# Optimization experiments

Measured on AMD Instinct MI355X. Metric: run time of the kernel, lower is better.

Reference implementation:

```python
import jax, jax.numpy as jnp
import numpy as np

N_NODES = 50000
N_EDGES = 800000
IN_DIM = 256
HID = 32
HEADS = 8
OUT_DIM = 16
NEG_SLOPE = 0.2


def setup_inputs() -> dict:
    key = jax.random.key(0)
    ks = jax.random.split(key, 12)
    s = 0.05
    return {
        "emb": jax.random.normal(ks[0], (N_NODES, IN_DIM), jnp.float32),
        "src": jax.random.randint(ks[1], (N_EDGES,), 0, N_NODES),
        "dst": jax.random.randint(ks[2], (N_EDGES,), 0, N_NODES),
        "W1": jax.random.normal(ks[3], (IN_DIM, HEADS * HID), jnp.float32) * s,
        "attn_l1": jax.random.normal(ks[4], (HEADS, HID), jnp.float32) * s,
        "attn_r1": jax.random.normal(ks[5], (HEADS, HID), jnp.float32) * s,
        "bias1": jax.random.normal(ks[6], (HEADS * HID,), jnp.float32) * s,
        "W2": jax.random.normal(ks[7], (HEADS * HID, OUT_DIM), jnp.float32) * s,
        "attn_l2": jax.random.normal(ks[8], (1, OUT_DIM), jnp.float32) * s,
        "attn_r2": jax.random.normal(ks[9], (1, OUT_DIM), jnp.float32) * s,
        "bias2": jax.random.normal(ks[10], (OUT_DIM,), jnp.float32) * s,
    }


def gat_conv(x, src, dst, W, attn_l, attn_r, bias, n_heads, d_out):
    # x: [N, F_in] -> per-head projection h: [N, H, D]
    n = x.shape[0]
    h = (x @ W).reshape(n, n_heads, d_out)
    el = jnp.sum(h * attn_l, axis=-1)  # [N, H]
    er = jnp.sum(h * attn_r, axis=-1)  # [N, H]
    # edge scores with LeakyReLU (DGL negative_slope=0.2)
    e = jax.nn.leaky_relu(el[src] + er[dst], NEG_SLOPE)  # [E, H]
    # edge softmax over incoming edges of each destination node
    m = jax.ops.segment_max(e, dst, num_segments=n)  # [N, H]
    ee = jnp.exp(e - m[dst])
    denom = jax.ops.segment_sum(ee, dst, num_segments=n)  # [N, H]
    alpha = ee / denom[dst]  # [E, H]
    # weighted scatter-sum aggregation
    out = jax.ops.segment_sum(h[src] * alpha[:, :, None], dst, num_segments=n)  # [N, H, D]
    return out + bias.reshape(1, n_heads, d_out)


def reference(emb, src, dst, W1, attn_l1, attn_r1, bias1, W2, attn_l2, attn_r2, bias2):
    h = gat_conv(emb, src, dst, W1, attn_l1, attn_r1, bias1, HEADS, HID)  # [N, 8, 32]
    h = jax.nn.elu(h.reshape(N_NODES, HEADS * HID))  # [N, 256]
    out = gat_conv(h, src, dst, W2, attn_l2, attn_r2, bias2, 1, OUT_DIM)  # [N, 1, 16]
    return jnp.squeeze(out, axis=1)  # [N, 16]
```

## Files before the change

### kernel.cpp

```cpp
#include <hip/hip_runtime.h>
#include <math.h>

#define N_NODES 50000
#define N_EDGES 800000
#define NEG_SLOPE 0.2f

typedef __attribute__((ext_vector_type(8))) short bf16x8;
typedef __attribute__((ext_vector_type(4))) float f32x4;
typedef __attribute__((ext_vector_type(4))) _Float16 half4;

__device__ inline unsigned short f32_to_bf16_rn(float x) {
    unsigned u = __builtin_bit_cast(unsigned, x);
    unsigned r = u + 0x7fffu + ((u >> 16) & 1u);
    return (unsigned short)(r >> 16);
}
__device__ inline float bf16_bits_to_f32(unsigned short h) {
    unsigned u = ((unsigned)h) << 16;
    return __builtin_bit_cast(float, u);
}
__device__ inline void load_lds16(const void* g, void* l) {
    __builtin_amdgcn_global_load_lds(
        (const __attribute__((address_space(1))) void*)g,
        (__attribute__((address_space(3))) void*)l, 16, 0, 0);
}


__global__ void count_deg(const int* __restrict__ dst, int* __restrict__ deg) {
    int i = blockIdx.x * 256 + threadIdx.x;
    if (i < N_EDGES) atomicAdd(&deg[dst[i]], 1);
}

__global__ void scan_block(const int* __restrict__ deg, int* __restrict__ tmp,
                           int* __restrict__ bsum) {
    __shared__ int buf[256];
    int tid = threadIdx.x;
    int i = blockIdx.x * 256 + tid;
    int v = (i < N_NODES) ? deg[i] : 0;
    buf[tid] = v;
    __syncthreads();
    for (int off = 1; off < 256; off <<= 1) {
        int x = (tid >= off) ? buf[tid - off] : 0;
        __syncthreads();
        buf[tid] += x;
        __syncthreads();
    }
    if (i < N_NODES) tmp[i] = buf[tid];
    if (tid == 255) bsum[blockIdx.x] = buf[255];
}

__global__ void finalize_offs(const int* __restrict__ tmp, const int* __restrict__ deg,
                              const int* __restrict__ bsum, int* __restrict__ offs,
                              int* __restrict__ cursor, int nb) {
    __shared__ int red[256];
    int tid = threadIdx.x;
    int b = blockIdx.x;
    red[tid] = (tid < nb && tid < b) ? bsum[tid] : 0;
    __syncthreads();
    for (int off = 128; off > 0; off >>= 1) {
        if (tid < off) red[tid] += red[tid + off];
        __syncthreads();
    }
    int prefix = red[0];
    int i = b * 256 + tid;
    if (i < N_NODES) {
        int incl = tmp[i] + prefix;
        offs[i + 1] = incl;
        cursor[i] = incl - deg[i];
        if (i == 0) offs[0] = 0;
    }
}

__global__ void scatter_edges(const int* __restrict__ src, const int* __restrict__ dst,
                              int* __restrict__ cursor, int* __restrict__ src_csr) {
    int i = blockIdx.x * 256 + threadIdx.x;
    if (i < N_EDGES) {
        int p = atomicAdd(&cursor[dst[i]], 1);
        src_csr[p] = src[i];
    }
}


__global__ void convert_W1T(const float* __restrict__ W,
                            unsigned short* __restrict__ Th,
                            unsigned short* __restrict__ Tl) {
    int n = blockIdx.x;
    int k = threadIdx.x;
    float x = W[k * 256 + n];
    unsigned short h = f32_to_bf16_rn(x);
    float lo = x - bf16_bits_to_f32(h);
    size_t idx = ((size_t)(k >> 3) * 256 + n) * 8 + (k & 7);
    Th[idx] = h;
    Tl[idx] = f32_to_bf16_rn(lo);
}


__global__ __launch_bounds__(256) void gemm1_fused(const float* __restrict__ A,
                                                   const unsigned short* __restrict__ BTh,
                                                   const unsigned short* __restrict__ BTl,
                                                   const float* __restrict__ al,
                                                   const float* __restrict__ ar,
                                                   _Float16* __restrict__ C,
                                                   float* __restrict__ el,
                                                   float* __restrict__ er, int M) {
    __shared__ unsigned short Ah[4][64][8], Al[4][64][8];
    __shared__ unsigned short Bh[4][256][8], Bl[4][256][8];
    int tid = threadIdx.x;
    int lane = tid & 63, wave = tid >> 6;
    int kgl = lane >> 4, rl = lane & 15;
    int row0 = blockIdx.x * 64;

    f32x4 acc[4][4];
#pragma unroll
    for (int i = 0; i < 4; i++)
#pragma unroll
        for (int j = 0; j < 4; j++) acc[i][j] = (f32x4){0.f, 0.f, 0.f, 0.f};

    int rowA = tid >> 2, kgA = tid & 3;
    int grA = row0 + rowA;
    const float* pA = &A[(size_t)grA * 256 + kgA * 8];
    float4 x0 = make_float4(0.f, 0.f, 0.f, 0.f);
    float4 x1 = make_float4(0.f, 0.f, 0.f, 0.f);
    if (grA < M) {
        x0 = *reinterpret_cast<const float4*>(pA);
        x1 = *reinterpret_cast<const float4*>(pA + 4);
    }

    for (int step = 0; step < 8; step++) {
        int k0 = step * 32;
        {
            float xs[8] = {x0.x, x0.y, x0.z, x0.w, x1.x, x1.y, x1.z, x1.w};
            unsigned short hs[8], ls[8];
#pragma unroll
            for (int j = 0; j < 8; j++) {
                hs[j] = f32_to_bf16_rn(xs[j]);
                ls[j] = f32_to_bf16_rn(xs[j] - bf16_bits_to_f32(hs[j]));
            }
            *reinterpret_cast<bf16x8*>(&Ah[kgA][rowA][0]) = *reinterpret_cast<bf16x8*>(hs);
            *reinterpret_cast<bf16x8*>(&Al[kgA][rowA][0]) = *reinterpret_cast<bf16x8*>(ls);
        }
        int s0 = k0 >> 3;
#pragma unroll
        for (int i = 0; i < 4; i++) {
            load_lds16(&BTh[((size_t)(s0 + i) * 256 + tid) * 8], &Bh[i][wave << 6][0]);
            load_lds16(&BTl[((size_t)(s0 + i) * 256 + tid) * 8], &Bl[i][wave << 6][0]);
        }
        __syncthreads();
        if (step < 7 && grA < M) {
            x0 = *reinterpret_cast<const float4*>(pA + (step + 1) * 32);
            x1 = *reinterpret_cast<const float4*>(pA + (step + 1) * 32 + 4);
        }
        bf16x8 a_h[4], a_l[4];
#pragma unroll
        for (int mf = 0; mf < 4; mf++) {
            int row = mf * 16 + rl;
            a_h[mf] = *reinterpret_cast<bf16x8*>(&Ah[kgl][row][0]);
            a_l[mf] = *reinterpret_cast<bf16x8*>(&Al[kgl][row][0]);
        }
#pragma unroll
        for (int nf = 0; nf < 4; nf++) {
            int col = wave * 64 + nf * 16 + rl;
            bf16x8 bh = *reinterpret_cast<bf16x8*>(&Bh[kgl][col][0]);
            bf16x8 bl = *reinterpret_cast<bf16x8*>(&Bl[kgl][col][0]);
#pragma unroll
            for (int mf = 0; mf < 4; mf++) {
                acc[mf][nf] = __builtin_amdgcn_mfma_f32_16x16x32_bf16(a_h[mf], bh, acc[mf][nf], 0, 0, 0);
                acc[mf][nf] = __builtin_amdgcn_mfma_f32_16x16x32_bf16(a_h[mf], bl, acc[mf][nf], 0, 0, 0);
                acc[mf][nf] = __builtin_amdgcn_mfma_f32_16x16x32_bf16(a_l[mf], bh, acc[mf][nf], 0, 0, 0);
            }
        }
        __syncthreads();
    }
    float alv[4], arv[4];
#pragma unroll
    for (int nf = 0; nf < 4; nf++) {
        int c = wave * 64 + nf * 16 + rl;
        alv[nf] = al[c];
        arv[nf] = ar[c];
    }
#pragma unroll
    for (int mf = 0; mf < 4; mf++) {
#pragma unroll
        for (int rr = 0; rr < 4; rr++) {
            int grow = row0 + mf * 16 + (lane >> 4) * 4 + rr;
            bool ok = grow < M;
            if (ok) {
#pragma unroll
                for (int nf = 0; nf < 4; nf++) {
                    int gcol = wave * 64 + nf * 16 + rl;
                    C[(size_t)grow * 256 + gcol] = (_Float16)acc[mf][nf][rr];
                }
            }
            float e0 = acc[mf][0][rr] * alv[0] + acc[mf][1][rr] * alv[1];
            float e1 = acc[mf][2][rr] * alv[2] + acc[mf][3][rr] * alv[3];
            float f0 = acc[mf][0][rr] * arv[0] + acc[mf][1][rr] * arv[1];
            float f1 = acc[mf][2][rr] * arv[2] + acc[mf][3][rr] * arv[3];
#pragma unroll
            for (int off = 8; off >= 1; off >>= 1) {
                e0 += __shfl_down(e0, off, 16);
                e1 += __shfl_down(e1, off, 16);
                f0 += __shfl_down(f0, off, 16);
                f1 += __shfl_down(f1, off, 16);
            }
            if (rl == 0 && ok) {
                int h0 = wave * 2;
                el[grow * 8 + h0] = e0;
                el[grow * 8 + h0 + 1] = e1;
                er[grow * 8 + h0] = f0;
                er[grow * 8 + h0 + 1] = f1;
            }
        }
    }
}


__global__ __launch_bounds__(64) void agg1_fused(const int* __restrict__ offs,
                                                 const int* __restrict__ src_csr,
                                                 const float* __restrict__ el,
                                                 const float* __restrict__ er,
                                                 const _Float16* __restrict__ h1h,
                                                 const float* __restrict__ bias1,
                                                 _Float16* __restrict__ x2) {
    __shared__ float sc[64][8];
    int v = blockIdx.x;
    int t = threadIdx.x;
    int head = t >> 3, slot = t & 7;
    int start = offs[v], end = offs[v + 1];
    int deg = end - start;
    int ncache = (deg < 64) ? deg : 64;
    float erv = er[v * 8 + head];
    float s = 0.f;
    for (int base = 0; base < ncache; base += 8) {
        int e = base + slot;
        if (e < ncache) {
            int u = src_csr[start + e];
            float x = el[u * 8 + head] + erv;
            x = (x >= 0.f) ? x : NEG_SLOPE * x;
            float ex = expf(x);
            sc[e][head] = ex;
            s += ex;
        }
    }
    for (int base = 64; base < deg; base += 8) {
        int e = base + slot;
        if (e < deg) {
            int u = src_csr[start + e];
            float x = el[u * 8 + head] + erv;
            x = (x >= 0.f) ? x : NEG_SLOPE * x;
            s += expf(x);
        }
    }
    s += __shfl_xor(s, 1);
    s += __shfl_xor(s, 2);
    s += __shfl_xor(s, 4);
    float invs = (s > 0.f) ? 1.f / s : 0.f;
    __syncthreads();
    float4 acc = make_float4(0.f, 0.f, 0.f, 0.f);
    int i = start;
    for (; i + 3 < end && (i - start) + 3 < 64; i += 4) {
        int e = i - start;
        int u0 = src_csr[i];
        int u1 = src_csr[i + 1];
        int u2 = src_csr[i + 2];
        int u3 = src_csr[i + 3];
        float a0 = sc[e][head] * invs;
        float a1 = sc[e + 1][head] * invs;
        float a2 = sc[e + 2][head] * invs;
        float a3 = sc[e + 3][head] * invs;
        half4 p0 = *reinterpret_cast<const half4*>(&h1h[(size_t)u0 * 256 + 4 * t]);
        half4 p1 = *reinterpret_cast<const half4*>(&h1h[(size_t)u1 * 256 + 4 * t]);
        half4 p2 = *reinterpret_cast<const half4*>(&h1h[(size_t)u2 * 256 + 4 * t]);
        half4 p3 = *reinterpret_cast<const half4*>(&h1h[(size_t)u3 * 256 + 4 * t]);
        acc.x += a0 * (float)p0[0] + a1 * (float)p1[0] + a2 * (float)p2[0] + a3 * (float)p3[0];
        acc.y += a0 * (float)p0[1] + a1 * (float)p1[1] + a2 * (float)p2[1] + a3 * (float)p3[1];
        acc.z += a0 * (float)p0[2] + a1 * (float)p1[2] + a2 * (float)p2[2] + a3 * (float)p3[2];
        acc.w += a0 * (float)p0[3] + a1 * (float)p1[3] + a2 * (float)p2[3] + a3 * (float)p3[3];
    }
    for (; i < end; i++) {
        int e = i - start;
        int u0 = src_csr[i];
        float a0;
        if (e < 64) {
            a0 = sc[e][head] * invs;
        } else {
            float x = el[u0 * 8 + head] + erv;
            x = (x >= 0.f) ? x : NEG_SLOPE * x;
            a0 = expf(x) * invs;
        }
        half4 p0 = *reinterpret_cast<const half4*>(&h1h[(size_t)u0 * 256 + 4 * t]);
        acc.x += a0 * (float)p0[0];
        acc.y += a0 * (float)p0[1];
        acc.z += a0 * (float)p0[2];
        acc.w += a0 * (float)p0[3];
    }
    float4 b = *reinterpret_cast<const float4*>(&bias1[4 * t]);
    float ox = acc.x + b.x, oy = acc.y + b.y, oz = acc.z + b.z, ow = acc.w + b.w;
    ox = (ox > 0.f) ? ox : (expf(ox) - 1.f);
    oy = (oy > 0.f) ? oy : (expf(oy) - 1.f);
    oz = (oz > 0.f) ? oz : (expf(oz) - 1.f);
    ow = (ow > 0.f) ? ow : (expf(ow) - 1.f);
    half4 o = {(_Float16)ox, (_Float16)oy, (_Float16)oz, (_Float16)ow};
    *reinterpret_cast<half4*>(&x2[(size_t)v * 256 + 4 * t]) = o;
}


__global__ __launch_bounds__(256) void gemm2_mfma(const _Float16* __restrict__ X,
                                                  const float* __restrict__ W2,
                                                  const float* __restrict__ al,
                                                  const float* __restrict__ ar,
                                                  float* __restrict__ h2,
                                                  float* __restrict__ el2,
                                                  float* __restrict__ er2, int M) {
    __shared__ unsigned short Xh[16][64][8], Xl[16][64][8];
    __shared__ unsigned short Wh[32][16][8], Wl[32][16][8];
    int tid = threadIdx.x;
    int lane = tid & 63, wave = tid >> 6;
    int kgl = lane >> 4, rl = lane & 15;
    int row0 = blockIdx.x * 64;

#pragma unroll
    for (int j = 0; j < 16; j++) {
        int e = tid * 16 + j;
        float x = W2[e];
        unsigned short h = f32_to_bf16_rn(x);
        unsigned short l = f32_to_bf16_rn(x - bf16_bits_to_f32(h));
        int k = e >> 4, c = e & 15;
        Wh[k >> 3][c][k & 7] = h;
        Wl[k >> 3][c][k & 7] = l;
    }

    f32x4 acc = (f32x4){0.f, 0.f, 0.f, 0.f};
    int rowX = tid >> 2, kgb = (tid & 3) * 4;
    int grX = row0 + rowX;
    for (int step = 0; step < 2; step++) {
#pragma unroll
        for (int j = 0; j < 4; j++) {
            int kg = kgb + j;
            int kglob = step * 128 + kg * 8;
            unsigned short hs[8], ls[8];
            if (grX < M) {
                half4 a0 = *reinterpret_cast<const half4*>(&X[(size_t)grX * 256 + kglob]);
                half4 a1 = *reinterpret_cast<const half4*>(&X[(size_t)grX * 256 + kglob + 4]);
                float xs[8] = {(float)a0[0], (float)a0[1], (float)a0[2], (float)a0[3],
                               (float)a1[0], (float)a1[1], (float)a1[2], (float)a1[3]};
#pragma unroll
                for (int q = 0; q < 8; q++) {
                    hs[q] = f32_to_bf16_rn(xs[q]);
                    ls[q] = f32_to_bf16_rn(xs[q] - bf16_bits_to_f32(hs[q]));
                }
            } else {
#pragma unroll
                for (int q = 0; q < 8; q++) { hs[q] = 0; ls[q] = 0; }
            }
            *reinterpret_cast<bf16x8*>(&Xh[kg][rowX][0]) = *reinterpret_cast<bf16x8*>(hs);
            *reinterpret_cast<bf16x8*>(&Xl[kg][rowX][0]) = *reinterpret_cast<bf16x8*>(ls);
        }
        __syncthreads();
#pragma unroll
        for (int ks = 0; ks < 4; ks++) {
            int kg = ks * 4 + kgl;
            int kgw = step * 16 + kg;
            bf16x8 a_h = *reinterpret_cast<bf16x8*>(&Xh[kg][wave * 16 + rl][0]);
            bf16x8 a_l = *reinterpret_cast<bf16x8*>(&Xl[kg][wave * 16 + rl][0]);
            bf16x8 b_h = *reinterpret_cast<bf16x8*>(&Wh[kgw][rl][0]);
            bf16x8 b_l = *reinterpret_cast<bf16x8*>(&Wl[kgw][rl][0]);
            acc = __builtin_amdgcn_mfma_f32_16x16x32_bf16(a_h, b_h, acc, 0, 0, 0);
            acc = __builtin_amdgcn_mfma_f32_16x16x32_bf16(a_h, b_l, acc, 0, 0, 0);
            acc = __builtin_amdgcn_mfma_f32_16x16x32_bf16(a_l, b_h, acc, 0, 0, 0);
        }
        __syncthreads();
    }
    float alv = al[rl], arv = ar[rl];
#pragma unroll
    for (int rr = 0; rr < 4; rr++) {
        int grow = row0 + wave * 16 + (lane >> 4) * 4 + rr;
        bool ok = grow < M;
        if (ok) h2[(size_t)grow * 16 + rl] = acc[rr];
        float pl = acc[rr] * alv;
        float pr = acc[rr] * arv;
#pragma unroll
        for (int off = 8; off >= 1; off >>= 1) {
            pl += __shfl_down(pl, off, 16);
            pr += __shfl_down(pr, off, 16);
        }
        if (rl == 0 && ok) {
            el2[grow] = pl;
            er2[grow] = pr;
        }
    }
}


__global__ __launch_bounds__(64) void agg2_fused(const int* __restrict__ offs,
                                                 const int* __restrict__ src_csr,
                                                 const float* __restrict__ el2,
                                                 const float* __restrict__ er2,
                                                 const float* __restrict__ h2,
                                                 const float* __restrict__ bias2,
                                                 float* __restrict__ out) {
    __shared__ float sc2[64];
    int v = blockIdx.x;
    int t = threadIdx.x;
    int start = offs[v], end = offs[v + 1];
    int deg = end - start;
    int ncache = (deg < 64) ? deg : 64;
    float erv = er2[v];
    float s = 0.f;
    for (int e = t; e < ncache; e += 64) {
        int u = src_csr[start + e];
        float x = el2[u] + erv;
        x = (x >= 0.f) ? x : NEG_SLOPE * x;
        float ex = expf(x);
        sc2[e] = ex;
        s += ex;
    }
    for (int e = 64 + t; e < deg; e += 64) {
        int u = src_csr[start + e];
        float x = el2[u] + erv;
        x = (x >= 0.f) ? x : NEG_SLOPE * x;
        s += expf(x);
    }
#pragma unroll
    for (int off = 32; off >= 1; off >>= 1) s += __shfl_xor(s, off);
    float invs = (s > 0.f) ? 1.f / s : 0.f;
    __syncthreads();
    int eg = t >> 4, d = t & 15;
    float acc = 0.f;
    for (int i = start + eg; i < end; i += 4) {
        int e = i - start;
        int u = src_csr[i];
        float a;
        if (e < 64) {
            a = sc2[e] * invs;
        } else {
            float x = el2[u] + erv;
            x = (x >= 0.f) ? x : NEG_SLOPE * x;
            a = expf(x) * invs;
        }
        acc += a * h2[(size_t)u * 16 + d];
    }
    acc += __shfl_xor(acc, 32);
    acc += __shfl_xor(acc, 16);
    if (t < 16) out[(size_t)v * 16 + t] = acc + bias2[t];
}


extern "C" void kernel_launch(void* const* d_in, const int* in_sizes, int n_in,
                              void* d_out, int out_size, void* d_ws, size_t ws_size,
                              hipStream_t stream) {
    const float* emb   = (const float*)d_in[0];
    const int*   src   = (const int*)d_in[1];
    const int*   dst   = (const int*)d_in[2];
    const float* W1    = (const float*)d_in[3];
    const float* al1   = (const float*)d_in[4];
    const float* ar1   = (const float*)d_in[5];
    const float* bias1 = (const float*)d_in[6];
    const float* W2    = (const float*)d_in[7];
    const float* al2   = (const float*)d_in[8];
    const float* ar2   = (const float*)d_in[9];
    const float* bias2 = (const float*)d_in[10];
    float* out = (float*)d_out;

    char* ws = (char*)d_ws;
    auto alloc = [&](size_t bytes) -> void* {
        void* p = ws;
        ws += (bytes + 255) & ~(size_t)255;
        return p;
    };
    int* deg     = (int*)alloc(N_NODES * 4);
    int* cursor  = (int*)alloc(N_NODES * 4);
    int* offs    = (int*)alloc((N_NODES + 1) * 4);
    int* tmp     = (int*)alloc(N_NODES * 4);
    int* bsum    = (int*)alloc(256 * 4);
    int* src_csr = (int*)alloc(N_EDGES * 4);
    unsigned short* W1Th = (unsigned short*)alloc(256 * 256 * 2);
    unsigned short* W1Tl = (unsigned short*)alloc(256 * 256 * 2);
    _Float16* h1h = (_Float16*)alloc((size_t)N_NODES * 256 * 2);
    float* el1   = (float*)alloc(N_NODES * 8 * 4);
    float* er1   = (float*)alloc(N_NODES * 8 * 4);
    _Float16* x2h = (_Float16*)alloc((size_t)N_NODES * 256 * 2);
    float* h2    = (float*)alloc((size_t)N_NODES * 16 * 4);
    float* el2   = (float*)alloc(N_NODES * 4);
    float* er2   = (float*)alloc(N_NODES * 4);

    int nb = (N_NODES + 255) / 256;

    hipMemsetAsync(deg, 0, N_NODES * 4, stream);
    count_deg<<<(N_EDGES + 255) / 256, 256, 0, stream>>>(dst, deg);
    scan_block<<<nb, 256, 0, stream>>>(deg, tmp, bsum);
    finalize_offs<<<nb, 256, 0, stream>>>(tmp, deg, bsum, offs, cursor, nb);
    scatter_edges<<<(N_EDGES + 255) / 256, 256, 0, stream>>>(src, dst, cursor, src_csr);

    convert_W1T<<<256, 256, 0, stream>>>(W1, W1Th, W1Tl);
    gemm1_fused<<<(N_NODES + 63) / 64, 256, 0, stream>>>(emb, W1Th, W1Tl, al1, ar1,
                                                         h1h, el1, er1, N_NODES);
    agg1_fused<<<N_NODES, 64, 0, stream>>>(offs, src_csr, el1, er1, h1h, bias1, x2h);
    gemm2_mfma<<<(N_NODES + 63) / 64, 256, 0, stream>>>(x2h, W2, al2, ar2, h2, el2, er2, N_NODES);
    agg2_fused<<<N_NODES, 64, 0, stream>>>(offs, src_csr, el2, er2, h2, bias2, out);
}
```

Before: 255.2 us.

## Merge CSR build with GEMM1 halves into fewer co-scheduled kernels

Fuses the preprocessing kernels with GEMM1 work through block-index dispatch. Degree counting shares a launch with the W1 conversion. The offset assignment (now a single-pass block scan with an atomic global counter, so offsets are no longer in node order) shares a launch with the first half of GEMM1. The edge scatter shares a launch with the second half. This removes several launches and lets the latency-bound graph-building work overlap with GEMM compute. The aggregation kernels now read the degree array instead of offs[v+1], because the segments are not contiguous in node order. The cost is divergent block roles, GEMM LDS being allocated for the small blocks, and non-monotone CSR placement that may reduce locality.

```diff
diff --git a/kernel.cpp b/kernel.cpp
--- a/kernel.cpp
+++ b/kernel.cpp
@@ -25,65 +25,15 @@
 }
 
 
-__global__ void count_deg(const int* __restrict__ dst, int* __restrict__ deg) {
-    int i = blockIdx.x * 256 + threadIdx.x;
+__device__ __forceinline__ void count_body(int bb, const int* __restrict__ dst,
+                                           int* __restrict__ deg) {
+    int i = bb * 256 + threadIdx.x;
     if (i < N_EDGES) atomicAdd(&deg[dst[i]], 1);
 }
 
-__global__ void scan_block(const int* __restrict__ deg, int* __restrict__ tmp,
-                           int* __restrict__ bsum) {
-    __shared__ int buf[256];
-    int tid = threadIdx.x;
-    int i = blockIdx.x * 256 + tid;
-    int v = (i < N_NODES) ? deg[i] : 0;
-    buf[tid] = v;
-    __syncthreads();
-    for (int off = 1; off < 256; off <<= 1) {
-        int x = (tid >= off) ? buf[tid - off] : 0;
-        __syncthreads();
-        buf[tid] += x;
-        __syncthreads();
-    }
-    if (i < N_NODES) tmp[i] = buf[tid];
-    if (tid == 255) bsum[blockIdx.x] = buf[255];
-}
-
-__global__ void finalize_offs(const int* __restrict__ tmp, const int* __restrict__ deg,
-                              const int* __restrict__ bsum, int* __restrict__ offs,
-                              int* __restrict__ cursor, int nb) {
-    __shared__ int red[256];
-    int tid = threadIdx.x;
-    int b = blockIdx.x;
-    red[tid] = (tid < nb && tid < b) ? bsum[tid] : 0;
-    __syncthreads();
-    for (int off = 128; off > 0; off >>= 1) {
-        if (tid < off) red[tid] += red[tid + off];
-        __syncthreads();
-    }
-    int prefix = red[0];
-    int i = b * 256 + tid;
-    if (i < N_NODES) {
-        int incl = tmp[i] + prefix;
-        offs[i + 1] = incl;
-        cursor[i] = incl - deg[i];
-        if (i == 0) offs[0] = 0;
-    }
-}
-
-__global__ void scatter_edges(const int* __restrict__ src, const int* __restrict__ dst,
-                              int* __restrict__ cursor, int* __restrict__ src_csr) {
-    int i = blockIdx.x * 256 + threadIdx.x;
-    if (i < N_EDGES) {
-        int p = atomicAdd(&cursor[dst[i]], 1);
-        src_csr[p] = src[i];
-    }
-}
-
-
-__global__ void convert_W1T(const float* __restrict__ W,
-                            unsigned short* __restrict__ Th,
-                            unsigned short* __restrict__ Tl) {
-    int n = blockIdx.x;
+__device__ __forceinline__ void convert_body(int n, const float* __restrict__ W,
+                                             unsigned short* __restrict__ Th,
+                                             unsigned short* __restrict__ Tl) {
     int k = threadIdx.x;
     float x = W[k * 256 + n];
     unsigned short h = f32_to_bf16_rn(x);
@@ -93,21 +43,58 @@
     Tl[idx] = f32_to_bf16_rn(lo);
 }
 
-
-__global__ __launch_bounds__(256) void gemm1_fused(const float* __restrict__ A,
-                                                   const unsigned short* __restrict__ BTh,
-                                                   const unsigned short* __restrict__ BTl,
-                                                   const float* __restrict__ al,
-                                                   const float* __restrict__ ar,
-                                                   _Float16* __restrict__ C,
-                                                   float* __restrict__ el,
-                                                   float* __restrict__ er, int M) {
+__device__ __forceinline__ void assign_body(int bb, const int* __restrict__ deg,
+                                            int* __restrict__ offs,
+                                            int* __restrict__ cursor,
+                                            int* __restrict__ gcounter) {
+    __shared__ int buf[256];
+    __shared__ int base;
+    int tid = threadIdx.x;
+    int v = bb * 256 + tid;
+    int d = (v < N_NODES) ? deg[v] : 0;
+    buf[tid] = d;
+    __syncthreads();
+    for (int off = 1; off < 256; off <<= 1) {
+        int x = (tid >= off) ? buf[tid - off] : 0;
+        __syncthreads();
+        buf[tid] += x;
+        __syncthreads();
+    }
+    if (tid == 255) base = atomicAdd(gcounter, buf[255]);
+    __syncthreads();
+    if (v < N_NODES) {
+        int start = base + buf[tid] - d;
+        offs[v] = start;
+        cursor[v] = start;
+    }
+}
+
+__device__ __forceinline__ void scatter_body(int bb, const int* __restrict__ src,
+                                             const int* __restrict__ dst,
+                                             int* __restrict__ cursor,
+                                             int* __restrict__ src_csr) {
+    int i = bb * 256 + threadIdx.x;
+    if (i < N_EDGES) {
+        int p = atomicAdd(&cursor[dst[i]], 1);
+        src_csr[p] = src[i];
+    }
+}
+
+
+__device__ __forceinline__ void gemm1_body(int bb, const float* __restrict__ A,
+                                           const unsigned short* __restrict__ BTh,
+                                           const unsigned short* __restrict__ BTl,
+                                           const float* __restrict__ al,
+                                           const float* __restrict__ ar,
+                                           _Float16* __restrict__ C,
+                                           float* __restrict__ el,
+                                           float* __restrict__ er, int M) {
     __shared__ unsigned short Ah[4][64][8], Al[4][64][8];
     __shared__ unsigned short Bh[4][256][8], Bl[4][256][8];
     int tid = threadIdx.x;
     int lane = tid & 63, wave = tid >> 6;
     int kgl = lane >> 4, rl = lane & 15;
-    int row0 = blockIdx.x * 64;
+    int row0 = bb * 64;
 
     f32x4 acc[4][4];
 #pragma unroll
@@ -213,7 +200,53 @@
 }
 
 
+__global__ __launch_bounds__(256) void k_count_convert(const int* __restrict__ dst,
+                                                       int* __restrict__ deg,
+                                                       const float* __restrict__ W1,
+                                                       unsigned short* __restrict__ Th,
+                                                       unsigned short* __restrict__ Tl) {
+    int b = blockIdx.x;
+    if (b < 3125) count_body(b, dst, deg);
+    else convert_body(b - 3125, W1, Th, Tl);
+}
+
+__global__ __launch_bounds__(256) void k_gemmA_assign(const float* __restrict__ A,
+                                                      const unsigned short* __restrict__ BTh,
+                                                      const unsigned short* __restrict__ BTl,
+                                                      const float* __restrict__ al,
+                                                      const float* __restrict__ ar,
+                                                      _Float16* __restrict__ C,
+                                                      float* __restrict__ el,
+                                                      float* __restrict__ er, int M,
+                                                      const int* __restrict__ deg,
+                                                      int* __restrict__ offs,
+                                                      int* __restrict__ cursor,
+                                                      int* __restrict__ gcounter) {
+    int b = blockIdx.x;
+    if (b < 391) gemm1_body(b, A, BTh, BTl, al, ar, C, el, er, M);
+    else assign_body(b - 391, deg, offs, cursor, gcounter);
+}
+
+__global__ __launch_bounds__(256) void k_gemmB_scatter(const float* __restrict__ A,
+                                                       const unsigned short* __restrict__ BTh,
+                                                       const unsigned short* __restrict__ BTl,
+                                                       const float* __restrict__ al,
+                                                       const float* __restrict__ ar,
+                                                       _Float16* __restrict__ C,
+                                                       float* __restrict__ el,
+                                                       float* __restrict__ er, int M,
+                                                       const int* __restrict__ src,
+                                                       const int* __restrict__ dst,
+                                                       int* __restrict__ cursor,
+                                                       int* __restrict__ src_csr) {
+    int b = blockIdx.x;
+    if (b < 391) gemm1_body(391 + b, A, BTh, BTl, al, ar, C, el, er, M);
+    else scatter_body(b - 391, src, dst, cursor, src_csr);
+}
+
+
 __global__ __launch_bounds__(64) void agg1_fused(const int* __restrict__ offs,
+                                                 const int* __restrict__ deg_arr,
                                                  const int* __restrict__ src_csr,
                                                  const float* __restrict__ el,
                                                  const float* __restrict__ er,
@@ -224,8 +257,9 @@
     int v = blockIdx.x;
     int t = threadIdx.x;
     int head = t >> 3, slot = t & 7;
-    int start = offs[v], end = offs[v + 1];
-    int deg = end - start;
+    int start = offs[v];
+    int deg = deg_arr[v];
+    int end = start + deg;
     int ncache = (deg < 64) ? deg : 64;
     float erv = er[v * 8 + head];
     float s = 0.f;
@@ -391,6 +425,7 @@
 
 
 __global__ __launch_bounds__(64) void agg2_fused(const int* __restrict__ offs,
+                                                 const int* __restrict__ deg_arr,
                                                  const int* __restrict__ src_csr,
                                                  const float* __restrict__ el2,
                                                  const float* __restrict__ er2,
@@ -400,8 +435,9 @@
     __shared__ float sc2[64];
     int v = blockIdx.x;
     int t = threadIdx.x;
-    int start = offs[v], end = offs[v + 1];
-    int deg = end - start;
+    int start = offs[v];
+    int deg = deg_arr[v];
+    int end = start + deg;
     int ncache = (deg < 64) ? deg : 64;
     float erv = er2[v];
     float s = 0.f;
@@ -466,11 +502,10 @@
         ws += (bytes + 255) & ~(size_t)255;
         return p;
     };
-    int* deg     = (int*)alloc(N_NODES * 4);
+    int* deg     = (int*)alloc((N_NODES + 64) * 4);
+    int* gcounter = deg + N_NODES;
     int* cursor  = (int*)alloc(N_NODES * 4);
-    int* offs    = (int*)alloc((N_NODES + 1) * 4);
-    int* tmp     = (int*)alloc(N_NODES * 4);
-    int* bsum    = (int*)alloc(256 * 4);
+    int* offs    = (int*)alloc(N_NODES * 4);
     int* src_csr = (int*)alloc(N_EDGES * 4);
     unsigned short* W1Th = (unsigned short*)alloc(256 * 256 * 2);
     unsigned short* W1Tl = (unsigned short*)alloc(256 * 256 * 2);
@@ -482,18 +517,13 @@
     float* el2   = (float*)alloc(N_NODES * 4);
     float* er2   = (float*)alloc(N_NODES * 4);
 
-    int nb = (N_NODES + 255) / 256;
-
-    hipMemsetAsync(deg, 0, N_NODES * 4, stream);
-    count_deg<<<(N_EDGES + 255) / 256, 256, 0, stream>>>(dst, deg);
-    scan_block<<<nb, 256, 0, stream>>>(deg, tmp, bsum);
-    finalize_offs<<<nb, 256, 0, stream>>>(tmp, deg, bsum, offs, cursor, nb);
-    scatter_edges<<<(N_EDGES + 255) / 256, 256, 0, stream>>>(src, dst, cursor, src_csr);
-
-    convert_W1T<<<256, 256, 0, stream>>>(W1, W1Th, W1Tl);
-    gemm1_fused<<<(N_NODES + 63) / 64, 256, 0, stream>>>(emb, W1Th, W1Tl, al1, ar1,
-                                                         h1h, el1, er1, N_NODES);
-    agg1_fused<<<N_NODES, 64, 0, stream>>>(offs, src_csr, el1, er1, h1h, bias1, x2h);
+    hipMemsetAsync(deg, 0, (N_NODES + 1) * 4, stream);
+    k_count_convert<<<3381, 256, 0, stream>>>(dst, deg, W1, W1Th, W1Tl);
+    k_gemmA_assign<<<587, 256, 0, stream>>>(emb, W1Th, W1Tl, al1, ar1, h1h, el1, er1,
+                                            N_NODES, deg, offs, cursor, gcounter);
+    k_gemmB_scatter<<<3516, 256, 0, stream>>>(emb, W1Th, W1Tl, al1, ar1, h1h, el1, er1,
+                                              N_NODES, src, dst, cursor, src_csr);
+    agg1_fused<<<N_NODES, 64, 0, stream>>>(offs, deg, src_csr, el1, er1, h1h, bias1, x2h);
     gemm2_mfma<<<(N_NODES + 63) / 64, 256, 0, stream>>>(x2h, W2, al2, ar2, h2, el2, er2, N_NODES);
-    agg2_fused<<<N_NODES, 64, 0, stream>>>(offs, src_csr, el2, er2, h2, bias2, out);
-}
+    agg2_fused<<<N_NODES, 64, 0, stream>>>(offs, deg, src_csr, el2, er2, h2, bias2, out);
+}
```

New measurement: 222.1 us. 1.15x faster.
